# Kernel optimization log

Hardware: AMD Instinct MI355X
Metric: run time of the kernel (lower is better)

Reference implementation:

```python
import jax, jax.numpy as jnp
import numpy as np

EPS = 1e-5
K_PATCHES = 5000  # sample_pixels // 16


def _resize_bilinear(x, h, w):
    # matches torch F.interpolate(mode='bilinear', align_corners=False)
    return jax.image.resize(x, (x.shape[0], x.shape[1], h, w), method="bilinear", antialias=False)


def _bn(x, g, b, m, v):
    # eval-mode BatchNorm2d with running stats
    inv = jax.lax.rsqrt(v + EPS)
    return (x - m[None, :, None, None]) * (g * inv)[None, :, None, None] + b[None, :, None, None]


def _conv(x, w):
    return jax.lax.conv_general_dilated(x, w, (1, 1), "VALID",
                                        dimension_numbers=("NCHW", "OIHW", "NCHW"))


def setup_inputs():
    key = jax.random.key(0)
    ks = jax.random.split(key, 14)
    B, Hc, Wc = 2, 512, 512
    pha = jax.random.uniform(ks[0], (B, 1, Hc, Wc), jnp.float32)
    err = jax.random.uniform(ks[1], (B, 1, Hc, Wc), jnp.float32)  # strictly >0 so mask is all-ones
    hid = jax.random.normal(ks[2], (B, 32, Hc, Wc), jnp.float32)

    def conv_w(k, o, i):
        return jax.random.normal(k, (o, i, 3, 3), jnp.float32) * 0.05

    def bn_p(k, c):
        k1, k2 = jax.random.split(k)
        return (1.0 + 0.1 * jax.random.normal(k1, (c,), jnp.float32),
                0.1 * jax.random.normal(k2, (c,), jnp.float32),
                jnp.zeros((c,), jnp.float32), jnp.ones((c,), jnp.float32))

    g1, b1, m1, v1 = bn_p(ks[4], 24)
    g2, b2, m2, v2 = bn_p(ks[6], 16)
    g3, b3, m3, v3 = bn_p(ks[8], 12)
    return dict(pha=pha, err=err, hid=hid,
                w1=conv_w(ks[3], 24, 33), g1=g1, b1=b1, m1=m1, v1=v1,
                w2=conv_w(ks[5], 16, 24), g2=g2, b2=b2, m2=m2, v2=v2,
                w3=conv_w(ks[7], 12, 16), g3=g3, b3=b3, m3=m3, v3=v3,
                w4=conv_w(ks[9], 1, 12),
                b4=0.1 * jax.random.normal(ks[10], (1,), jnp.float32),
                H_full=2048, W_full=2048)


def reference(pha, err, hid, w1, g1, b1, m1, v1, w2, g2, b2, m2, v2,
              w3, g3, b3, m3, v3, w4, b4, H_full, W_full):
    B = pha.shape[0]
    Hh, Wh = H_full // 2, W_full // 2
    Hq, Wq = H_full // 4, W_full // 4

    # --- select_refinement_regions (sampling mode) ---
    err_q = _resize_bilinear(err, Hq, Wq)                      # (B,1,Hq,Wq)
    flat = err_q.reshape(B, -1)
    _, top_idx = jax.lax.top_k(flat, K_PATCHES)                # (B,K)
    ref = jnp.zeros_like(flat).at[jnp.arange(B)[:, None], top_idx].set(1.0)
    ref = ref * (flat > 0).astype(flat.dtype)                  # prevent_oversampling
    ref = ref.reshape(B, 1, Hq, Wq)

    # nonzero(ref) == topk locations here (err is strictly positive)
    bidx = jnp.repeat(jnp.arange(B), K_PATCHES)                # (P,)
    hidx = (top_idx // Wq).reshape(-1)                         # (P,)
    widx = (top_idx % Wq).reshape(-1)                          # (P,)

    # --- crop_patch (unfold-equivalent gather), size=2, padding=3 ---
    x = jnp.concatenate([hid, pha], axis=1)                    # (B,33,Hc,Wc)
    x = _resize_bilinear(x, Hh, Wh)                            # (B,33,Hh,Wh)
    pad, size = 3, 2
    win = size + 2 * pad                                       # 8
    xp = jnp.pad(x, ((0, 0), (0, 0), (pad, pad), (pad, pad)))
    rows = hidx[:, None] * size + jnp.arange(win)              # (P,8)
    cols = widx[:, None] * size + jnp.arange(win)              # (P,8)
    patches = xp[bidx[:, None, None], :, rows[:, :, None], cols[:, None, :]]  # (P,8,8,33)
    patches = patches.transpose(0, 3, 1, 2)                    # (P,33,8,8)

    # --- small conv stack ---
    y = jax.nn.relu(_bn(_conv(patches, w1), g1, b1, m1, v1))   # (P,24,6,6)
    y = jax.nn.relu(_bn(_conv(y, w2), g2, b2, m2, v2))         # (P,16,4,4)
    y = jnp.repeat(jnp.repeat(y, 2, axis=2), 2, axis=3)        # nearest -> (P,16,8,8)
    y = jax.nn.relu(_bn(_conv(y, w3), g3, b3, m3, v3))         # (P,12,6,6)
    y = _conv(y, w4) + b4[None, :, None, None]                 # (P,1,4,4)

    # --- replace_patch (scatter_nd of 4x4 blocks into full-res pha) ---
    pha_full = _resize_bilinear(pha, H_full, W_full)           # (B,1,H,W)
    pr = hidx[:, None, None] * 4 + jnp.arange(4)[None, :, None]  # (P,4,1)
    pc = widx[:, None, None] * 4 + jnp.arange(4)[None, None, :]  # (P,1,4)
    pha_full = pha_full.at[bidx[:, None, None], 0, pr, pc].set(y[:, 0])
    return pha_full, ref
```

## Files before the change

### kernel.cpp

```cpp
#include <hip/hip_runtime.h>
#include <stdint.h>

#define K_SEL 5000
#define NQ    262144
#define NB    2

#define BIAS_OFF 38912
#define W4_OFF   39424
#define ST_OFF   40960

#define WS_HIST  16
#define WS_SEL   2064
#define WS_EQ    12064
#define EQ_CAP   4096
#define WS_BCNT  20480
#define WS_BBASE 21504

typedef _Float16 f16x8 __attribute__((ext_vector_type(8)));
typedef _Float16 f16x4 __attribute__((ext_vector_type(4)));
typedef float    f32x4 __attribute__((ext_vector_type(4)));
#define MFMA16(a,b,c) __builtin_amdgcn_mfma_f32_16x16x32_f16(a,b,c,0,0,0)

__global__ void prep_kernel(const float* __restrict__ w1, const float* __restrict__ g1,
                            const float* __restrict__ b1, const float* __restrict__ m1,
                            const float* __restrict__ v1,
                            const float* __restrict__ w2, const float* __restrict__ g2,
                            const float* __restrict__ b2, const float* __restrict__ m2,
                            const float* __restrict__ v2,
                            const float* __restrict__ w3, const float* __restrict__ g3,
                            const float* __restrict__ b3, const float* __restrict__ m3,
                            const float* __restrict__ v3,
                            const float* __restrict__ w4, const float* __restrict__ b4,
                            char* __restrict__ ws) {
    _Float16* wf = (_Float16*)ws;
    float* bias = (float*)(ws + BIAS_OFF);
    float* w4r  = (float*)(ws + W4_OFF);
    uint32_t* st = (uint32_t*)(ws + ST_OFF);
    int tid = threadIdx.x;
    for (int t = tid; t < 38 * 512; t += 256) {
        int frag = t >> 9, li = (t >> 3) & 63, j = t & 7;
        int lo = li & 15, hi = li >> 4;
        float val = 0.f;
        if (frag < 18) {
            int ky = frag / 6, r = frag % 6, kx = r >> 1, mt = r & 1;
            int oc = mt * 16 + lo, ci = hi * 8 + j;
            if (oc < 24) val = w1[((oc * 33 + ci) * 3 + ky) * 3 + kx] * g1[oc] * rsqrtf(v1[oc] + 1e-5f);
        } else if (frag < 27) {
            int f = frag - 18, ky = f / 3, kt = f % 3;
            int oc = lo, k = kt * 32 + hi * 8 + j;
            if (k < 72) {
                int kx = k / 24, ci = k % 24;
                val = w2[((oc * 24 + ci) * 3 + ky) * 3 + kx] * g2[oc] * rsqrtf(v2[oc] + 1e-5f);
            }
        } else if (frag < 36) {
            int s = frag - 27, ky = s / 3, kx = s % 3;
            int oc = lo, ci = hi * 8 + j;
            if (oc < 12 && ci < 16) val = w3[((oc * 16 + ci) * 3 + ky) * 3 + kx] * g3[oc] * rsqrtf(v3[oc] + 1e-5f);
        } else {
            int mt = frag - 36, oc = mt * 16 + lo, tap = hi * 8 + j;
            if (oc < 24 && tap < 9)
                val = w1[((oc * 33 + 32) * 3 + tap / 3) * 3 + tap % 3] * g1[oc] * rsqrtf(v1[oc] + 1e-5f);
        }
        wf[t] = (_Float16)val;
    }
    if (tid < 53) {
        float v;
        if (tid < 24)      { float sc = g1[tid] * rsqrtf(v1[tid] + 1e-5f); v = b1[tid] - m1[tid] * sc; }
        else if (tid < 40) { int c = tid - 24; float sc = g2[c] * rsqrtf(v2[c] + 1e-5f); v = b2[c] - m2[c] * sc; }
        else if (tid < 52) { int c = tid - 40; float sc = g3[c] * rsqrtf(v3[c] + 1e-5f); v = b3[c] - m3[c] * sc; }
        else v = b4[0];
        bias[tid] = v;
    }
    if (tid < 144) { int t9 = tid / 16, ci = tid % 16; w4r[tid] = (ci < 12) ? w4[ci * 9 + t9] : 0.f; }
    for (int i = tid; i < WS_HIST + 4 * 512; i += 256) st[i] = 0u;
    __syncthreads();
    if (tid == 0) { st[2] = K_SEL; st[3] = K_SEL; }
}

__global__ void hist_kernel(const float* __restrict__ err, uint32_t* st, int round) {
    __shared__ uint32_t h[256];
    h[threadIdx.x] = 0u;
    __syncthreads();
    int t = blockIdx.x * 256 + threadIdx.x;
    int b = t >> 18;
    uint32_t bits = __float_as_uint(err[t]);
    uint32_t pref = st[b];
    int shift = 24 - 8 * round;
    bool match = (round == 0) || ((bits >> (shift + 8)) == (pref >> (shift + 8)));
    if (match) atomicAdd(&h[(bits >> shift) & 255u], 1u);
    __syncthreads();
    uint32_t v = h[threadIdx.x];
    if (v) atomicAdd(&st[WS_HIST + round * 512 + b * 256 + threadIdx.x], v);
}

__global__ void scan_kernel(uint32_t* st, int round) {
    int b = blockIdx.x;
    int lane = threadIdx.x;
    int shift = 24 - 8 * round;
    const uint32_t* hist = st + WS_HIST + round * 512 + b * 256;
    int binbase = 255 - 4 * lane;
    uint32_t hv0 = hist[binbase], hv1 = hist[binbase - 1],
             hv2 = hist[binbase - 2], hv3 = hist[binbase - 3];
    uint32_t p = hv0 + hv1 + hv2 + hv3;
    uint32_t cum = p;
    for (int o = 1; o < 64; o <<= 1) {
        uint32_t n = __shfl_up(cum, o);
        if (lane >= o) cum += n;
    }
    uint32_t rem = st[2 + b];
    unsigned long long bal = __ballot(cum >= rem);
    int first = __ffsll(bal) - 1;
    if (lane == first) {
        uint32_t acc = cum - p;
        uint32_t hv[4] = {hv0, hv1, hv2, hv3};
        int chosen = binbase;
        for (int q = 0; q < 4; q++) {
            if (acc + hv[q] >= rem) { chosen = binbase - q; break; }
            acc += hv[q];
        }
        uint32_t pref = st[b] | ((uint32_t)chosen << shift);
        st[b] = pref;
        st[2 + b] = rem - acc;
        if (round == 3) { st[4 + b] = pref; st[6 + b] = rem - acc; }
    }
}

__global__ void ccount_kernel(const float* __restrict__ err, uint32_t* st) {
    __shared__ uint32_t wsum[8];
    int blk = blockIdx.x, tid = threadIdx.x;
    int b = blk >> 9, base = (blk & 511) << 9;
    uint32_t T = st[4 + b];
    uint32_t b0 = __float_as_uint(err[b * NQ + base + tid]);
    uint32_t b1 = __float_as_uint(err[b * NQ + base + 256 + tid]);
    unsigned long long m0 = __ballot(b0 > T);
    unsigned long long m1 = __ballot(b1 > T);
    int w = tid >> 6, lane = tid & 63;
    if (lane == 0) { wsum[w] = (uint32_t)__popcll(m0); wsum[4 + w] = (uint32_t)__popcll(m1); }
    __syncthreads();
    if (tid == 0)
        st[WS_BCNT + blk] = wsum[0] + wsum[1] + wsum[2] + wsum[3]
                          + wsum[4] + wsum[5] + wsum[6] + wsum[7];
}

__global__ void cscan_kernel(uint32_t* st) {
    __shared__ uint32_t wtot[8];
    int b = blockIdx.x, tid = threadIdx.x;
    int lane = tid & 63, w = tid >> 6;
    uint32_t v = st[WS_BCNT + b * 512 + tid];
    uint32_t inc = v;
    for (int o = 1; o < 64; o <<= 1) {
        uint32_t n = __shfl_up(inc, o);
        if (lane >= o) inc += n;
    }
    if (lane == 63) wtot[w] = inc;
    __syncthreads();
    uint32_t off = 0;
    for (int j = 0; j < w; j++) off += wtot[j];
    uint32_t base = off + inc - v;
    st[WS_BBASE + b * 512 + tid] = base;
    if (tid == 511) st[8 + b] = base + v;
}

__global__ void cplace_kernel(const float* __restrict__ err, uint32_t* st,
                              float* __restrict__ refout) {
    __shared__ uint32_t wc[8];
    int blk = blockIdx.x, tid = threadIdx.x;
    int b = blk >> 9, base = (blk & 511) << 9;
    uint32_t T = st[4 + b];
    uint32_t blkbase = st[WS_BBASE + b * 512 + (blk & 511)];
    int i0 = base + tid, i1 = base + 256 + tid;
    uint32_t b0 = __float_as_uint(err[b * NQ + i0]);
    uint32_t b1 = __float_as_uint(err[b * NQ + i1]);
    bool s0 = b0 > T, s1 = b1 > T;
    unsigned long long m0 = __ballot(s0);
    unsigned long long m1 = __ballot(s1);
    int w = tid >> 6, lane = tid & 63;
    if (lane == 0) { wc[w] = (uint32_t)__popcll(m0); wc[4 + w] = (uint32_t)__popcll(m1); }
    refout[b * NQ + i0] = s0 ? 1.0f : 0.0f;
    refout[b * NQ + i1] = s1 ? 1.0f : 0.0f;
    __syncthreads();
    uint32_t tot0 = wc[0] + wc[1] + wc[2] + wc[3];
    uint32_t pre0 = 0, pre1 = tot0;
    for (int j = 0; j < w; j++) { pre0 += wc[j]; pre1 += wc[4 + j]; }
    unsigned long long lt = (1ull << lane) - 1ull;
    if (s0) {
        uint32_t slot = blkbase + pre0 + (uint32_t)__popcll(m0 & lt);
        if (slot < K_SEL) st[WS_SEL + b * K_SEL + slot] = (uint32_t)i0;
    }
    if (s1) {
        uint32_t slot = blkbase + pre1 + (uint32_t)__popcll(m1 & lt);
        if (slot < K_SEL) st[WS_SEL + b * K_SEL + slot] = (uint32_t)i1;
    }
    if (b0 == T) { uint32_t e = atomicAdd(&st[10 + b], 1u); if (e < EQ_CAP) st[WS_EQ + b * EQ_CAP + e] = (uint32_t)i0; }
    if (b1 == T) { uint32_t e = atomicAdd(&st[10 + b], 1u); if (e < EQ_CAP) st[WS_EQ + b * EQ_CAP + e] = (uint32_t)i1; }
}

__global__ void select_kernel(uint32_t* st, float* __restrict__ refout) {
    __shared__ uint32_t L[EQ_CAP];
    int b = blockIdx.x;
    uint32_t m = st[10 + b]; if (m > EQ_CAP) m = EQ_CAP;
    uint32_t need = st[6 + b];
    uint32_t T = st[4 + b];
    for (uint32_t j = threadIdx.x; j < m; j += blockDim.x) L[j] = st[WS_EQ + b * EQ_CAP + j];
    __syncthreads();
    for (uint32_t j = threadIdx.x; j < m; j += blockDim.x) {
        uint32_t idx = L[j];
        uint32_t rank = 0;
        for (uint32_t q = 0; q < m; q++) rank += (L[q] < idx) ? 1u : 0u;
        if (rank < need) {
            uint32_t slot = atomicAdd(&st[8 + b], 1u);
            if (slot < K_SEL) st[WS_SEL + b * K_SEL + slot] = idx;
            refout[b * NQ + idx] = (T != 0u) ? 1.0f : 0.0f;
        }
    }
}

__global__ void upsample_kernel(const float* __restrict__ pha, float* __restrict__ out) {
    int t = blockIdx.x * 256 + threadIdx.x;
    int xq = t & 511;
    int rest = t >> 9;
    int oy = rest & 2047;
    int b  = rest >> 11;
    const float* src = pha + (size_t)b * NQ;
    float sy = oy * 0.25f - 0.375f;
    sy = fminf(fmaxf(sy, 0.0f), 511.0f);
    int y0 = (int)sy; int y1i = min(y0 + 1, 511);
    float fy = sy - (float)y0;
    float rv[4];
#pragma unroll
    for (int j = 0; j < 4; j++) {
        int ox = xq * 4 + j;
        float sx = ox * 0.25f - 0.375f;
        sx = fminf(fmaxf(sx, 0.0f), 511.0f);
        int x0 = (int)sx; int x1i = min(x0 + 1, 511);
        float fx = sx - (float)x0;
        float v00 = src[y0 * 512 + x0],  v01 = src[y0 * 512 + x1i];
        float v10 = src[y1i * 512 + x0], v11 = src[y1i * 512 + x1i];
        rv[j] = v00 * (1.f - fy) * (1.f - fx) + v01 * (1.f - fy) * fx
              + v10 * fy * (1.f - fx)         + v11 * fy * fx;
    }
    float4 r4 = make_float4(rv[0], rv[1], rv[2], rv[3]);
    *reinterpret_cast<float4*>(out + (size_t)b * 4194304 + (size_t)oy * 2048 + xq * 4) = r4;
}

__device__ __forceinline__ f16x8 ldfrag(const _Float16* wf, int frag, int l) {
    return *(const f16x8*)(wf + frag * 512 + l * 8);
}

__global__ __launch_bounds__(128) void patch_kernel(
    const float* __restrict__ hid, const float* __restrict__ pha,
    const char* __restrict__ ws, float* __restrict__ out) {
    __shared__ _Float16 xs[64][40];
    __shared__ _Float16 y1n[36][40];
    __shared__ _Float16 pool[64][40];
    __shared__ float pha8[64];
    __shared__ float biasL[56];
    float* y3s = (float*)&y1n[0][0];

    const _Float16* wf = (const _Float16*)ws;
    const float* biasG = (const float*)(ws + BIAS_OFF);
    const float* w4r   = (const float*)(ws + W4_OFF);
    const uint32_t* st = (const uint32_t*)(ws + ST_OFF);

    int tid = threadIdx.x, l = tid & 63, wid = tid >> 6;
    int lo = l & 15, hi = l >> 4;
    int bp = blockIdx.x;
    int b = (bp >= K_SEL) ? 1 : 0;
    int pi = bp - b * K_SEL;
    uint32_t idx = st[WS_SEL + b * K_SEL + pi] & 0x3FFFFu;
    int hq = (int)(idx >> 9), wq = (int)(idx & 511u);

    if (tid < 53) biasL[tid] = biasG[tid];

    int ry = l >> 3, rx = l & 7;
    int hy = hq * 2 + ry - 3, hx = wq * 2 + rx - 3;
    bool inb = ((unsigned)hy < 1024u) && ((unsigned)hx < 1024u);
    float sy = fminf(fmaxf(hy * 0.5f - 0.25f, 0.f), 511.f);
    float sx = fminf(fmaxf(hx * 0.5f - 0.25f, 0.f), 511.f);
    int y0 = (int)sy, x0 = (int)sx;
    int y1c = min(y0 + 1, 511), x1c = min(x0 + 1, 511);
    float fy = sy - (float)y0, fx = sx - (float)x0;
    int o00 = y0 * 512 + x0, o01 = y0 * 512 + x1c, o10 = y1c * 512 + x0, o11 = y1c * 512 + x1c;
    float w00 = (1.f - fy) * (1.f - fx), w01 = (1.f - fy) * fx;
    float w10 = fy * (1.f - fx), w11 = fy * fx;

    _Float16 hv[16];
    {
        const float* hb = hid + ((size_t)b * 32 + wid * 16) * NQ;
#pragma unroll
        for (int c = 0; c < 16; c++) {
            const float* p = hb + (size_t)c * NQ;
            float v = 0.f;
            if (inb) v = p[o00] * w00 + p[o01] * w01 + p[o10] * w10 + p[o11] * w11;
            hv[c] = (_Float16)v;
        }
    }
    f16x8 h0 = {hv[0], hv[1], hv[2], hv[3], hv[4], hv[5], hv[6], hv[7]};
    f16x8 h1 = {hv[8], hv[9], hv[10], hv[11], hv[12], hv[13], hv[14], hv[15]};
    {
        _Float16* xrow = &xs[l][wid * 16];
        *(f16x8*)xrow = h0;
        *((f16x8*)xrow + 1) = h1;
    }
    f16x8 z8 = {(_Float16)0.f, (_Float16)0.f, (_Float16)0.f, (_Float16)0.f,
                (_Float16)0.f, (_Float16)0.f, (_Float16)0.f, (_Float16)0.f};
    if (wid == 1) {
        const float* p = pha + (size_t)b * NQ;
        float v = 0.f;
        if (inb) v = p[o00] * w00 + p[o01] * w01 + p[o10] * w10 + p[o11] * w11;
        pha8[l] = v;
    }
    __syncthreads();

    if (wid == 0) {
        if (l < 48) {
            int py = (l * 43) >> 8, px = l - py * 6;
            _Float16 tap[9];
#pragma unroll
            for (int t = 0; t < 9; t++) {
                int ky = t / 3, kx = t % 3;
                int ip = (py + ky) * 8 + px + kx;
                tap[t] = (_Float16)pha8[ip & 63];
            }
            _Float16* row = &pool[l][0];
            f16x8 r0 = {tap[0], tap[1], tap[2], tap[3], tap[4], tap[5], tap[6], tap[7]};
            f16x8 r1 = z8; r1[0] = tap[8];
            *(f16x8*)row = r0;
            *(f16x8*)(row + 8)  = r1;
            *(f16x8*)(row + 16) = z8;
            *(f16x8*)(row + 24) = z8;
        }
    } else {
        for (int i = l; i < 72; i += 64) {
            *(f16x8*)&y1n[i >> 1][24 + (i & 1) * 8] = z8;
        }
    }
    __syncthreads();

    f32x4 zf = {0.f, 0.f, 0.f, 0.f};
    f32x4 aA0 = zf, aA1 = zf, aB = zf;
    int nA = wid * 16 + lo, nB = 32 + lo;
    int pyA = (nA * 43) >> 8, pxA = nA - pyA * 6;
    int pyB = (nB * 43) >> 8, pxB = nB - pyB * 6;
    {
        f16x8 A0 = ldfrag(wf, 36, l), A1 = ldfrag(wf, 37, l);
        f16x8 BA = *(const f16x8*)&pool[nA][hi * 8];
        f16x8 BB = *(const f16x8*)&pool[nB][hi * 8];
        aA0 = MFMA16(A0, BA, aA0);
        aA1 = MFMA16(A1, BA, aA1);
        aB  = MFMA16(wid ? A1 : A0, BB, aB);
    }
#pragma unroll
    for (int ky = 0; ky < 3; ky++) {
#pragma unroll
        for (int kt = 0; kt < 3; kt++) {
            f16x8 A0 = ldfrag(wf, ky * 6 + kt * 2 + 0, l);
            f16x8 A1 = ldfrag(wf, ky * 6 + kt * 2 + 1, l);
            int rA = ((pyA + ky) * 8 + pxA + kt) & 63;
            int rB = ((pyB + ky) * 8 + pxB + kt) & 63;
            f16x8 BA = *(const f16x8*)&xs[rA][hi * 8];
            f16x8 BB = *(const f16x8*)&xs[rB][hi * 8];
            aA0 = MFMA16(A0, BA, aA0);
            aA1 = MFMA16(A1, BA, aA1);
            aB  = MFMA16(wid ? A1 : A0, BB, aB);
        }
    }
    {
        f32x4 accs[3] = {aA0, aA1, aB};
        int mts[3] = {0, 1, wid};
        int nts[3] = {wid, wid, 2};
#pragma unroll
        for (int f = 0; f < 3; f++) {
            int n = nts[f] * 16 + lo;
            int ocb = mts[f] * 16 + hi * 4;
            if (n < 36 && ocb < 24) {
                f16x4 hh;
                hh[0] = (_Float16)fmaxf(accs[f][0] + biasL[ocb + 0], 0.f);
                hh[1] = (_Float16)fmaxf(accs[f][1] + biasL[ocb + 1], 0.f);
                hh[2] = (_Float16)fmaxf(accs[f][2] + biasL[ocb + 2], 0.f);
                hh[3] = (_Float16)fmaxf(accs[f][3] + biasL[ocb + 3], 0.f);
                *(f16x4*)&y1n[n][ocb] = hh;
            }
        }
    }
    __syncthreads();

    if (wid == 0) {
        f32x4 a2 = zf;
        int qy = lo >> 2, qx = lo & 3;
#pragma unroll
        for (int ky = 0; ky < 3; ky++) {
#pragma unroll
            for (int kt = 0; kt < 3; kt++) {
                f16x8 A = ldfrag(wf, 18 + ky * 3 + kt, l);
                int k = kt * 32 + hi * 8;
                const _Float16* bptr;
                if (k < 72) {
                    int kx = k / 24, ci0 = k - kx * 24;
                    bptr = &y1n[(qy + ky) * 6 + qx + kx][ci0];
                } else {
                    bptr = &y1n[0][24];
                }
                f16x8 B = *(const f16x8*)bptr;
                a2 = MFMA16(A, B, a2);
            }
        }
        int ocb = hi * 4;
        f16x4 hh;
        hh[0] = (_Float16)fmaxf(a2[0] + biasL[24 + ocb + 0], 0.f);
        hh[1] = (_Float16)fmaxf(a2[1] + biasL[24 + ocb + 1], 0.f);
        hh[2] = (_Float16)fmaxf(a2[2] + biasL[24 + ocb + 2], 0.f);
        hh[3] = (_Float16)fmaxf(a2[3] + biasL[24 + ocb + 3], 0.f);
#pragma unroll
        for (int dy = 0; dy < 2; dy++)
#pragma unroll
            for (int dx = 0; dx < 2; dx++) {
                int row = (2 * qy + dy) * 8 + 2 * qx + dx;
                *(f16x4*)&pool[row][ocb] = hh;
            }
    } else {
        *(f16x8*)&pool[l][16] = z8;
        *(f16x8*)&pool[l][24] = z8;
    }
    __syncthreads();

    f32x4 aC = zf, aD = zf;
    int nC = wid * 16 + lo, nD = 32 + lo;
    int pyC = (nC * 43) >> 8, pxC = nC - pyC * 6;
    int pyD = (nD * 43) >> 8, pxD = nD - pyD * 6;
#pragma unroll
    for (int s = 0; s < 9; s++) {
        int ky = s / 3, kx = s % 3;
        f16x8 A = ldfrag(wf, 27 + s, l);
        f16x8 BC = *(const f16x8*)&pool[((pyC + ky) * 8 + pxC + kx) & 63][hi * 8];
        aC = MFMA16(A, BC, aC);
        if (wid) {
            f16x8 BD = *(const f16x8*)&pool[((pyD + ky) * 8 + pxD + kx) & 63][hi * 8];
            aD = MFMA16(A, BD, aD);
        }
    }
    __syncthreads();
    {
        int ocb = hi * 4;
        f32x4 accs[2] = {aC, aD};
        int nts[2] = {wid, 2};
        int cnt = wid ? 2 : 1;
        for (int f = 0; f < cnt; f++) {
            int n = nts[f] * 16 + lo;
            if (n < 36) {
                f32x4 v;
#pragma unroll
                for (int r = 0; r < 4; r++) {
                    float bb = (ocb + r < 12) ? biasL[40 + ocb + r] : 0.f;
                    float x = accs[f][r] + bb;
                    v[r] = (ocb + r < 12) ? fmaxf(x, 0.f) : 0.f;
                }
                *(f32x4*)&y3s[n * 16 + ocb] = v;
            }
        }
    }
    __syncthreads();

    if (wid == 0) {
        int r4 = lo >> 2, c4 = lo & 3, cig = hi;
        float acc = 0.f;
#pragma unroll
        for (int t = 0; t < 9; t++) {
            int ky = t / 3, kx = t % 3;
            const f32x4 xv = *(const f32x4*)&y3s[((r4 + ky) * 6 + c4 + kx) * 16 + cig * 4];
            const f32x4 wv = *(const f32x4*)(w4r + t * 16 + cig * 4);
            acc += xv[0] * wv[0] + xv[1] * wv[1] + xv[2] * wv[2] + xv[3] * wv[3];
        }
        acc += __shfl_xor(acc, 32);
        acc += __shfl_xor(acc, 16);
        if (l < 16) {
            out[(size_t)b * 4194304 + (size_t)(hq * 4 + r4) * 2048 + (wq * 4 + c4)] = acc + biasL[52];
        }
    }
}

extern "C" void kernel_launch(void* const* d_in, const int* in_sizes, int n_in,
                              void* d_out, int out_size, void* d_ws, size_t ws_size,
                              hipStream_t stream) {
    const float* pha = (const float*)d_in[0];
    const float* err = (const float*)d_in[1];
    const float* hid = (const float*)d_in[2];
    const float* w1  = (const float*)d_in[3];
    const float* g1  = (const float*)d_in[4];
    const float* bb1 = (const float*)d_in[5];
    const float* m1  = (const float*)d_in[6];
    const float* v1  = (const float*)d_in[7];
    const float* w2  = (const float*)d_in[8];
    const float* g2  = (const float*)d_in[9];
    const float* bb2 = (const float*)d_in[10];
    const float* m2  = (const float*)d_in[11];
    const float* v2  = (const float*)d_in[12];
    const float* w3  = (const float*)d_in[13];
    const float* g3  = (const float*)d_in[14];
    const float* bb3 = (const float*)d_in[15];
    const float* m3  = (const float*)d_in[16];
    const float* v3  = (const float*)d_in[17];
    const float* w4  = (const float*)d_in[18];
    const float* b4  = (const float*)d_in[19];

    float* out    = (float*)d_out;
    float* refout = out + (size_t)NB * 4194304;
    char* ws      = (char*)d_ws;
    uint32_t* st  = (uint32_t*)(ws + ST_OFF);

    prep_kernel<<<1, 256, 0, stream>>>(w1, g1, bb1, m1, v1, w2, g2, bb2, m2, v2,
                                       w3, g3, bb3, m3, v3, w4, b4, ws);
    for (int r = 0; r < 4; r++) {
        hist_kernel<<<2048, 256, 0, stream>>>(err, st, r);
        scan_kernel<<<2, 64, 0, stream>>>(st, r);
    }
    ccount_kernel<<<1024, 256, 0, stream>>>(err, st);
    cscan_kernel<<<2, 512, 0, stream>>>(st);
    cplace_kernel<<<1024, 256, 0, stream>>>(err, st, refout);
    select_kernel<<<2, 256, 0, stream>>>(st, refout);
    upsample_kernel<<<8192, 256, 0, stream>>>(pha, out);
    patch_kernel<<<2 * K_SEL, 128, 0, stream>>>(hid, pha, ws, out);
}
```

Baseline: 158.7 us.

## Pre-transpose hidden features to channel-last fp16 for patch gathers

Adds a pass that converts the 32-channel hidden map plus alpha into a channel-last fp16 buffer (40 halves per pixel) in workspace. The patch kernel then gathers each bilinear tap with two 16-byte vector loads instead of 16 strided scalar loads across channel planes. The cost is an extra full-tensor read of about 67MB and a write of about 42MB every call, which may outweigh the gather savings for only 10000 patches. The new path runs only when the workspace is large enough; otherwise the old gather path is kept.

```diff
diff --git a/kernel.cpp b/kernel.cpp
--- a/kernel.cpp
+++ b/kernel.cpp
@@ -8,6 +8,9 @@
 #define BIAS_OFF 38912
 #define W4_OFF   39424
 #define ST_OFF   40960
+#define XT_OFF   131072
+#define XT_BYTES ((size_t)NB * NQ * 40 * 2)
+#define WS_NEED  (XT_OFF + XT_BYTES)
 
 #define WS_HIST  16
 #define WS_SEL   2064
@@ -77,6 +80,22 @@
     if (tid == 0) { st[2] = K_SEL; st[3] = K_SEL; }
 }
 
+__global__ void transpose_kernel(const float* __restrict__ hid, const float* __restrict__ pha,
+                                 _Float16* __restrict__ xt) {
+    int t = blockIdx.x * 256 + threadIdx.x;
+    int b = t >> 18, i = t & (NQ - 1);
+    _Float16 v[40];
+#pragma unroll
+    for (int c = 0; c < 32; c++)
+        v[c] = (_Float16)hid[((size_t)(b * 32 + c)) * NQ + i];
+    v[32] = (_Float16)pha[(size_t)b * NQ + i];
+#pragma unroll
+    for (int c = 33; c < 40; c++) v[c] = (_Float16)0.f;
+    _Float16* dst = xt + (size_t)t * 40;
+#pragma unroll
+    for (int q = 0; q < 5; q++) *(f16x8*)(dst + q * 8) = *(const f16x8*)(v + q * 8);
+}
+
 __global__ void hist_kernel(const float* __restrict__ err, uint32_t* st, int round) {
     __shared__ uint32_t h[256];
     h[threadIdx.x] = 0u;
@@ -247,8 +266,10 @@
     return *(const f16x8*)(wf + frag * 512 + l * 8);
 }
 
+template<bool XT>
 __global__ __launch_bounds__(128) void patch_kernel(
     const float* __restrict__ hid, const float* __restrict__ pha,
+    const _Float16* __restrict__ xt,
     const char* __restrict__ ws, float* __restrict__ out) {
     __shared__ _Float16 xs[64][40];
     __shared__ _Float16 y1n[36][40];
@@ -285,7 +306,29 @@
     float w10 = fy * (1.f - fx), w11 = fy * fx;
 
     _Float16 hv[16];
-    {
+    if (XT) {
+        if (inb) {
+            const _Float16* xtb = xt + (size_t)b * NQ * 40 + (size_t)wid * 16;
+            const _Float16* p00 = xtb + (size_t)o00 * 40;
+            const _Float16* p01 = xtb + (size_t)o01 * 40;
+            const _Float16* p10 = xtb + (size_t)o10 * 40;
+            const _Float16* p11 = xtb + (size_t)o11 * 40;
+            f16x8 a0 = *(const f16x8*)p00, a1 = *(const f16x8*)(p00 + 8);
+            f16x8 b0 = *(const f16x8*)p01, b1 = *(const f16x8*)(p01 + 8);
+            f16x8 c0 = *(const f16x8*)p10, c1 = *(const f16x8*)(p10 + 8);
+            f16x8 d0 = *(const f16x8*)p11, d1 = *(const f16x8*)(p11 + 8);
+#pragma unroll
+            for (int j = 0; j < 8; j++) {
+                hv[j]     = (_Float16)(w00 * (float)a0[j] + w01 * (float)b0[j]
+                                     + w10 * (float)c0[j] + w11 * (float)d0[j]);
+                hv[j + 8] = (_Float16)(w00 * (float)a1[j] + w01 * (float)b1[j]
+                                     + w10 * (float)c1[j] + w11 * (float)d1[j]);
+            }
+        } else {
+#pragma unroll
+            for (int c = 0; c < 16; c++) hv[c] = (_Float16)0.f;
+        }
+    } else {
         const float* hb = hid + ((size_t)b * 32 + wid * 16) * NQ;
 #pragma unroll
         for (int c = 0; c < 16; c++) {
@@ -507,9 +550,13 @@
     float* refout = out + (size_t)NB * 4194304;
     char* ws      = (char*)d_ws;
     uint32_t* st  = (uint32_t*)(ws + ST_OFF);
+    _Float16* xt  = (_Float16*)(ws + XT_OFF);
+    bool use_xt   = (ws_size >= WS_NEED);
 
     prep_kernel<<<1, 256, 0, stream>>>(w1, g1, bb1, m1, v1, w2, g2, bb2, m2, v2,
                                        w3, g3, bb3, m3, v3, w4, b4, ws);
+    if (use_xt)
+        transpose_kernel<<<2048, 256, 0, stream>>>(hid, pha, xt);
     for (int r = 0; r < 4; r++) {
         hist_kernel<<<2048, 256, 0, stream>>>(err, st, r);
         scan_kernel<<<2, 64, 0, stream>>>(st, r);
@@ -519,5 +566,8 @@
     cplace_kernel<<<1024, 256, 0, stream>>>(err, st, refout);
     select_kernel<<<2, 256, 0, stream>>>(st, refout);
     upsample_kernel<<<8192, 256, 0, stream>>>(pha, out);
-    patch_kernel<<<2 * K_SEL, 128, 0, stream>>>(hid, pha, ws, out);
-}
+    if (use_xt)
+        patch_kernel<true><<<2 * K_SEL, 128, 0, stream>>>(hid, pha, xt, ws, out);
+    else
+        patch_kernel<false><<<2 * K_SEL, 128, 0, stream>>>(hid, pha, xt, ws, out);
+}
```

Measured after the change: 156.3 us. Within noise of the previous version (-1.5%).
